# Performance work log

Measured on AMD Instinct MI355X. Metric: run time of the kernel, lower is better.

The kernel has to match this reference:

```python
import jax, jax.numpy as jnp
import numpy as np

EMBED = 1024
HEADS = 16
HEAD_DIM = EMBED // HEADS
WIN = 256  # attention_window w; band width = 2w+1


def setup_inputs() -> dict:
    key = jax.random.key(0)
    ks = jax.random.split(key, 10)
    b, s, e = 2, 4096, EMBED
    scale = 1.0 / np.sqrt(e)
    inp = {"x": jax.random.normal(ks[0], (b, s, e), jnp.float32)}
    for i, (wn, bn) in enumerate([("Wq", "bq"), ("Wk", "bk"), ("Wv", "bv"), ("Wo", "bo")]):
        inp[wn] = jax.random.normal(ks[1 + i], (e, e), jnp.float32) * scale
        inp[bn] = jax.random.normal(ks[5 + i], (e,), jnp.float32) * 0.01
    return inp


def _rope_headaxis(x):
    # Replicates RotaryEmbedding applied to [b, s, h, d]: the original indexes
    # x.shape[2] (== num_heads here), so phase varies over the HEAD axis.
    h, d = x.shape[2], x.shape[3]
    inv = 1.0 / (10000.0 ** (jnp.arange(0, d, 2, dtype=jnp.float32) / d))
    freqs = jnp.arange(h, dtype=jnp.float32)[:, None] * inv[None, :]
    emb = jnp.concatenate([freqs, freqs], axis=-1)  # [h, d]
    cos = jnp.cos(emb)[None, None]  # [1,1,h,d]
    sin = jnp.sin(emb)[None, None]
    x2 = jnp.stack([-x[..., 1::2], x[..., 0::2]], axis=-1).reshape(x.shape)
    return x * cos + x2 * sin


def reference(x, Wq, bq, Wk, bk, Wv, bv, Wo, bo):
    b, s, e = x.shape
    h, d, w = HEADS, HEAD_DIM, WIN
    q = (x @ Wq.T + bq).reshape(b, s, h, d)
    k = (x @ Wk.T + bk).reshape(b, s, h, d)
    v = (x @ Wv.T + bv).reshape(b, s, h, d)
    q = _rope_headaxis(q) / jnp.sqrt(jnp.float32(d))
    k = _rope_headaxis(k)

    # Band (sliding-window) attention: query chunk c of size w attends to key
    # chunks c-1, c, c+1 (3w keys); relative-position + boundary masking makes
    # this identical to the original sliding_chunks band of width 2w+1.
    nc = s // w
    qc = q.reshape(b, nc, w, h, d)
    pad = [(0, 0), (w, w), (0, 0), (0, 0)]
    kp = jnp.pad(k, pad)
    vp = jnp.pad(v, pad)
    idx = jnp.arange(nc)[:, None] * w + jnp.arange(3 * w)[None, :]  # [nc, 3w]
    k3 = kp[:, idx]  # [b, nc, 3w, h, d]
    v3 = vp[:, idx]
    scores = jnp.einsum('bcxhd,bcyhd->bhcxy', qc, k3)  # [b,h,nc,w,3w]

    c = jnp.arange(nc)[:, None, None]
    xq = jnp.arange(w)[None, :, None]
    y = jnp.arange(3 * w)[None, None, :]
    kpos = c * w + y - w  # absolute key position
    valid = (y >= xq) & (y <= xq + 2 * w) & (kpos >= 0) & (kpos < s)
    scores = jnp.where(valid[None, None], scores, -jnp.inf)

    probs = jax.nn.softmax(scores, axis=-1)  # fp32 softmax, as in original
    ctx = jnp.einsum('bhcxy,bcyhd->bcxhd', probs, v3).reshape(b, s, e)
    return ctx @ Wo.T + bo
```

## Files before the change

kernel.cpp:

```cpp
#include <hip/hip_runtime.h>


typedef _Float16 half8 __attribute__((ext_vector_type(8)));
typedef _Float16 half4v __attribute__((ext_vector_type(4)));
typedef float floatx4 __attribute__((ext_vector_type(4)));

typedef __attribute__((address_space(3))) unsigned int lds_u32;
typedef const __attribute__((address_space(1))) unsigned int glb_u32;

__device__ __forceinline__ void async_copy16(const void* g, void* l) {
  __builtin_amdgcn_global_load_lds((glb_u32*)g, (lds_u32*)l, 16, 0, 0);
}

__global__ __launch_bounds__(256) void convert_kernel(
    const float* __restrict__ x, const float* __restrict__ wq,
    const float* __restrict__ wk, const float* __restrict__ wv,
    const float* __restrict__ wo, _Float16* __restrict__ dst) {
  const int e0 = (blockIdx.x * 256 + threadIdx.x) * 4;
  const float* src; int off;
  if      (e0 <  8388608) { src = x;  off = e0; }
  else if (e0 <  9437184) { src = wq; off = e0 -  8388608; }
  else if (e0 < 10485760) { src = wk; off = e0 -  9437184; }
  else if (e0 < 11534336) { src = wv; off = e0 - 10485760; }
  else                    { src = wo; off = e0 - 11534336; }
  const float4 f = *(const float4*)(src + off);
  half4v h;
  h[0] = (_Float16)f.x; h[1] = (_Float16)f.y;
  h[2] = (_Float16)f.z; h[3] = (_Float16)f.w;
  *(half4v*)(dst + e0) = h;
}

__global__ __launch_bounds__(256, 2) void gemm_qkv_kernel(
    const _Float16* __restrict__ A, const _Float16* __restrict__ w0,
    const _Float16* __restrict__ w1, const _Float16* __restrict__ w2,
    const float* __restrict__ b0, const float* __restrict__ b1,
    const float* __restrict__ b2, _Float16* __restrict__ o0,
    _Float16* __restrict__ o1, _Float16* __restrict__ o2) {
  __shared__ _Float16 As[128 * 32];
  __shared__ _Float16 Bs[128 * 32];
  const int tid = threadIdx.x;
  const int w = tid >> 6, lane = tid & 63;
  const int l4 = lane & 15, quad = lane >> 4;
  const int wm = w & 1, wn = w >> 1;
  const int m0 = blockIdx.x * 128, n0 = blockIdx.y * 128;

  const _Float16* B; const float* bias; _Float16* out;
  if (blockIdx.z == 0)      { B = w0; bias = b0; out = o0; }
  else if (blockIdx.z == 1) { B = w1; bias = b1; out = o1; }
  else                      { B = w2; bias = b2; out = o2; }
  const bool dorope = blockIdx.z < 2;
  const float scl = (blockIdx.z == 0) ? 0.18033688f : 1.0f;

  const floatx4 zero = {0.f, 0.f, 0.f, 0.f};
  floatx4 acc[4][4];
#pragma unroll
  for (int i = 0; i < 4; ++i)
#pragma unroll
    for (int j = 0; j < 4; ++j) acc[i][j] = zero;

  const int fcb = (quad ^ ((l4 >> 2) & 3)) * 8;

  for (int kt = 0; kt < 32; ++kt) {
    const int k0 = kt * 32;
#pragma unroll
    for (int i = 0; i < 2; ++i) {
      const int p = i * 256 + tid;
      const int r = p >> 2;
      const int cb = (p & 3) ^ ((r >> 2) & 3);
      async_copy16(A + (m0 + r) * 1024 + k0 + cb * 8, As + (i * 256 + w * 64) * 8);
      async_copy16(B + (n0 + r) * 1024 + k0 + cb * 8, Bs + (i * 256 + w * 64) * 8);
    }
    __syncthreads();
    half8 af[4], bf[4];
#pragma unroll
    for (int mt = 0; mt < 4; ++mt)
      af[mt] = *(const half8*)(As + (wm * 64 + mt * 16 + l4) * 32 + fcb);
#pragma unroll
    for (int nt = 0; nt < 4; ++nt)
      bf[nt] = *(const half8*)(Bs + (wn * 64 + nt * 16 + l4) * 32 + fcb);
#pragma unroll
    for (int mt = 0; mt < 4; ++mt)
#pragma unroll
      for (int nt = 0; nt < 4; ++nt)
        acc[mt][nt] = __builtin_amdgcn_mfma_f32_16x16x32_f16(af[mt], bf[nt], acc[mt][nt], 0, 0, 0);
    __syncthreads();
  }

#pragma unroll
  for (int nt = 0; nt < 4; ++nt) {
    const int n = n0 + wn * 64 + nt * 16 + l4;
    const float bval = bias[n];
    const int hh = n >> 6, dd = n & 63;
    float c_ = 1.f, ss = 0.f;
    if (dorope) {
      const float freq = __expf((float)(n & 31) * -0.28782314f);
      float s_;
      __sincosf((float)hh * freq, &s_, &c_);
      ss = (n & 1) ? s_ : -s_;
    }
#pragma unroll
    for (int mt = 0; mt < 4; ++mt)
#pragma unroll
      for (int r = 0; r < 4; ++r) {
        const int m = m0 + wm * 64 + mt * 16 + quad * 4 + r;
        const int bb = m >> 12, s = m & 4095;
        float val = acc[mt][nt][r] + bval;
        const float prt = __shfl_xor(val, 1);
        if (dorope) val = (val * c_ + prt * ss) * scl;
        out[((bb * 16 + hh) * 4096 + s) * 64 + dd] = (_Float16)val;
      }
  }
}

__global__ __launch_bounds__(256, 2) void gemm_out_kernel(
    const _Float16* __restrict__ A, const _Float16* __restrict__ B,
    const float* __restrict__ bias, float* __restrict__ out) {
  __shared__ _Float16 As[128 * 32];
  __shared__ _Float16 Bs[128 * 32];
  const int tid = threadIdx.x;
  const int w = tid >> 6, lane = tid & 63;
  const int l4 = lane & 15, quad = lane >> 4;
  const int wm = w & 1, wn = w >> 1;
  const int m0 = blockIdx.x * 128, n0 = blockIdx.y * 128;

  const floatx4 zero = {0.f, 0.f, 0.f, 0.f};
  floatx4 acc[4][4];
#pragma unroll
  for (int i = 0; i < 4; ++i)
#pragma unroll
    for (int j = 0; j < 4; ++j) acc[i][j] = zero;

  const int fcb = (quad ^ ((l4 >> 2) & 3)) * 8;

  for (int kt = 0; kt < 32; ++kt) {
    const int k0 = kt * 32;
#pragma unroll
    for (int i = 0; i < 2; ++i) {
      const int p = i * 256 + tid;
      const int r = p >> 2;
      const int cb = (p & 3) ^ ((r >> 2) & 3);
      async_copy16(A + (m0 + r) * 1024 + k0 + cb * 8, As + (i * 256 + w * 64) * 8);
      async_copy16(B + (n0 + r) * 1024 + k0 + cb * 8, Bs + (i * 256 + w * 64) * 8);
    }
    __syncthreads();
    half8 af[4], bf[4];
#pragma unroll
    for (int mt = 0; mt < 4; ++mt)
      af[mt] = *(const half8*)(As + (wm * 64 + mt * 16 + l4) * 32 + fcb);
#pragma unroll
    for (int nt = 0; nt < 4; ++nt)
      bf[nt] = *(const half8*)(Bs + (wn * 64 + nt * 16 + l4) * 32 + fcb);
#pragma unroll
    for (int mt = 0; mt < 4; ++mt)
#pragma unroll
      for (int nt = 0; nt < 4; ++nt)
        acc[mt][nt] = __builtin_amdgcn_mfma_f32_16x16x32_f16(af[mt], bf[nt], acc[mt][nt], 0, 0, 0);
    __syncthreads();
  }

#pragma unroll
  for (int nt = 0; nt < 4; ++nt) {
    const int n = n0 + wn * 64 + nt * 16 + l4;
    const float bval = bias[n];
#pragma unroll
    for (int mt = 0; mt < 4; ++mt)
#pragma unroll
      for (int r = 0; r < 4; ++r) {
        const int m = m0 + wm * 64 + mt * 16 + quad * 4 + r;
        out[m * 1024 + n] = acc[mt][nt][r] + bval;
      }
  }
}

__global__ __launch_bounds__(256) void transpose_v(const _Float16* __restrict__ v,
                                                   _Float16* __restrict__ vt) {
  __shared__ _Float16 tile[64 * 70];
  const int t = threadIdx.x;
  const int bh = blockIdx.y, s0 = blockIdx.x * 64;
  const _Float16* src = v + (bh * 4096 + s0) * 64;
#pragma unroll
  for (int i = 0; i < 2; ++i) {
    const int c = i * 256 + t;
    const int row = c >> 3, cb = c & 7;
    const half8 d = *(const half8*)(src + row * 64 + cb * 8);
#pragma unroll
    for (int u = 0; u < 8; ++u) tile[(cb * 8 + u) * 70 + row] = d[u];
  }
  __syncthreads();
  _Float16* dst = vt + bh * 262144 + s0;
#pragma unroll
  for (int i = 0; i < 2; ++i) {
    const int c = i * 256 + t;
    const int dd = c >> 3, scb = c & 7;
    half8 d;
#pragma unroll
    for (int u = 0; u < 8; ++u) d[u] = tile[dd * 70 + scb * 8 + u];
    *(half8*)(dst + dd * 4096 + scb * 8) = d;
  }
}

__global__ __launch_bounds__(256, 2) void attn_kernel(
    const _Float16* __restrict__ qg, const _Float16* __restrict__ kg,
    const _Float16* __restrict__ vtg, _Float16* __restrict__ ctx) {
  __shared__ _Float16 Ks[128 * 64];
  __shared__ _Float16 Vs[64 * 128];

  const int tid = threadIdx.x;
  const int w = tid >> 6, lane = tid & 63;
  const int l4 = lane & 15, quad = lane >> 4;
  const int q0 = blockIdx.x * 128;
  const int bh = blockIdx.y;
  const _Float16* qbh = qg + bh * 262144;
  const _Float16* kbh = kg + bh * 262144;
  const _Float16* vbh = vtg + bh * 262144;

  half8 qf[2][2];
#pragma unroll
  for (int nt = 0; nt < 2; ++nt)
#pragma unroll
    for (int ks = 0; ks < 2; ++ks)
      qf[nt][ks] = *(const half8*)(qbh + (q0 + w * 32 + nt * 16 + l4) * 64 + ks * 32 + quad * 8);

  const floatx4 zero = {0.f, 0.f, 0.f, 0.f};
  floatx4 OT[4][2];
  float m_st[2], l_st[2];
#pragma unroll
  for (int md = 0; md < 4; ++md)
#pragma unroll
    for (int nt = 0; nt < 2; ++nt) OT[md][nt] = zero;
#pragma unroll
  for (int nt = 0; nt < 2; ++nt) { m_st[nt] = -1e30f; l_st[nt] = 0.f; }

  for (int t = 0; t < 5; ++t) {
    const int kv0 = q0 + (t - 2) * 128;
    if (kv0 < 0 || kv0 >= 4096) continue;

#pragma unroll
    for (int i = 0; i < 4; ++i) {
      const int p = i * 256 + tid;
      const int rk = p >> 3, ck = (p & 7) ^ (rk & 7);
      async_copy16(kbh + (kv0 + rk) * 64 + ck * 8, Ks + (i * 256 + w * 64) * 8);
      const int rv = p >> 4, cv = (p & 15) ^ (rv & 7);
      async_copy16(vbh + rv * 4096 + kv0 + cv * 8, Vs + (i * 256 + w * 64) * 8);
    }
    __syncthreads();

    const bool edge = (t == 0 || t == 4);
#pragma unroll
    for (int hf = 0; hf < 2; ++hf) {
      const int kb = hf * 64;

      floatx4 ST[4][2];
#pragma unroll
      for (int m = 0; m < 4; ++m)
#pragma unroll
        for (int nt = 0; nt < 2; ++nt) ST[m][nt] = zero;
#pragma unroll
      for (int ks = 0; ks < 2; ++ks)
#pragma unroll
        for (int m = 0; m < 4; ++m) {
          const half8 kf = *(const half8*)(Ks + (kb + m * 16 + l4) * 64 +
                                           ((ks * 4 + quad) ^ (l4 & 7)) * 8);
#pragma unroll
          for (int nt = 0; nt < 2; ++nt)
            ST[m][nt] = __builtin_amdgcn_mfma_f32_16x16x32_f16(kf, qf[nt][ks], ST[m][nt], 0, 0, 0);
        }

      if (edge) {
#pragma unroll
        for (int m = 0; m < 4; ++m)
#pragma unroll
          for (int r = 0; r < 4; ++r) {
            const int key = kv0 + kb + m * 16 + quad * 4 + r;
#pragma unroll
            for (int nt = 0; nt < 2; ++nt) {
              const int d = key - (q0 + w * 32 + nt * 16 + l4);
              if (d < -256 || d > 256) ST[m][nt][r] = -1e30f;
            }
          }
      }

#pragma unroll
      for (int nt = 0; nt < 2; ++nt) {
        float mx = -1e30f;
#pragma unroll
        for (int m = 0; m < 4; ++m)
#pragma unroll
          for (int r = 0; r < 4; ++r) mx = fmaxf(mx, ST[m][nt][r]);
        mx = fmaxf(mx, __shfl_xor(mx, 16));
        mx = fmaxf(mx, __shfl_xor(mx, 32));
        const float mnew = fmaxf(m_st[nt], mx);
        const float alpha = exp2f(m_st[nt] - mnew);
        m_st[nt] = mnew;
        float rs = 0.f;
#pragma unroll
        for (int m = 0; m < 4; ++m)
#pragma unroll
          for (int r = 0; r < 4; ++r) {
            const float pv = exp2f(ST[m][nt][r] - mnew);
            ST[m][nt][r] = pv;
            rs += pv;
          }
        rs += __shfl_xor(rs, 16);
        rs += __shfl_xor(rs, 32);
        l_st[nt] = l_st[nt] * alpha + rs;
#pragma unroll
        for (int md = 0; md < 4; ++md)
#pragma unroll
          for (int r = 0; r < 4; ++r) OT[md][nt][r] *= alpha;
      }

#pragma unroll
      for (int m = 0; m < 4; ++m) {
        half4v pb[2];
#pragma unroll
        for (int nt = 0; nt < 2; ++nt) {
          const auto lo = __builtin_amdgcn_cvt_pkrtz(ST[m][nt][0], ST[m][nt][1]);
          const auto hi = __builtin_amdgcn_cvt_pkrtz(ST[m][nt][2], ST[m][nt][3]);
          pb[nt][0] = (_Float16)lo[0]; pb[nt][1] = (_Float16)lo[1];
          pb[nt][2] = (_Float16)hi[0]; pb[nt][3] = (_Float16)hi[1];
        }
#pragma unroll
        for (int md = 0; md < 4; ++md) {
          const half4v vf = *(const half4v*)(Vs + (md * 16 + l4) * 128 +
                                             (((hf * 8 + m * 2 + (quad >> 1)) ^ (l4 & 7)) * 8 +
                                              (quad & 1) * 4));
#pragma unroll
          for (int nt = 0; nt < 2; ++nt)
            OT[md][nt] = __builtin_amdgcn_mfma_f32_16x16x16f16(vf, pb[nt], OT[md][nt], 0, 0, 0);
        }
      }
    }
    __syncthreads();
  }

  const int b = bh >> 4, hh = bh & 15;
#pragma unroll
  for (int nt = 0; nt < 2; ++nt) {
    const float inv_l = 1.f / l_st[nt];
    const int s = q0 + w * 32 + nt * 16 + l4;
#pragma unroll
    for (int md = 0; md < 4; ++md) {
      half4v o;
#pragma unroll
      for (int r = 0; r < 4; ++r) o[r] = (_Float16)(OT[md][nt][r] * inv_l);
      *(half4v*)(ctx + (b * 4096 + s) * 1024 + hh * 64 + md * 16 + quad * 4) = o;
    }
  }
}

extern "C" void kernel_launch(void* const* d_in, const int* in_sizes, int n_in,
                              void* d_out, int out_size, void* d_ws, size_t ws_size,
                              hipStream_t stream) {
  const float* x  = (const float*)d_in[0];
  const float* Wq = (const float*)d_in[1];
  const float* bq = (const float*)d_in[2];
  const float* Wk = (const float*)d_in[3];
  const float* bk = (const float*)d_in[4];
  const float* Wv = (const float*)d_in[5];
  const float* bv = (const float*)d_in[6];
  const float* Wo = (const float*)d_in[7];
  const float* bo = (const float*)d_in[8];

  _Float16* ws   = (_Float16*)d_ws;
  _Float16* xh   = ws;
  _Float16* wqh  = ws + 8388608;
  _Float16* wkh  = ws + 9437184;
  _Float16* wvh  = ws + 10485760;
  _Float16* woh  = ws + 11534336;
  _Float16* qh   = ws + 12582912;
  _Float16* kh   = ws + 20971520;
  _Float16* vh   = ws + 29360128;
  _Float16* vth  = ws + 37748736;
  _Float16* ctxh = xh;

  convert_kernel<<<12288, 256, 0, stream>>>(x, Wq, Wk, Wv, Wo, ws);
  gemm_qkv_kernel<<<dim3(64, 8, 3), 256, 0, stream>>>(xh, wqh, wkh, wvh,
                                                      bq, bk, bv, qh, kh, vh);
  transpose_v<<<dim3(64, 32), 256, 0, stream>>>(vh, vth);
  attn_kernel<<<dim3(32, 32), 256, 0, stream>>>(qh, kh, vth, ctxh);
  gemm_out_kernel<<<dim3(64, 8), 256, 0, stream>>>(ctxh, woh, bo, (float*)d_out);
}
```

Baseline: 258.4 us.

## Deepen GEMM K-tile, remap blocks per XCD, stage QKV epilogue through LDS

Both GEMMs now load 64-wide K slices (16 iterations instead of 32), which halves the barrier count, and use an XOR swizzle sized for 8 chunks. Blocks are linearized and remapped so that each XCD handles a contiguous group of M tiles, to improve L2 reuse of A and B. The QKV epilogue writes its results into padded LDS and then issues coalesced 16-byte stores into the head-major layout, replacing scattered 2-byte stores. LDS use per block grows to about 34 KB, which may limit occupancy.

```diff
diff --git a/kernel.cpp b/kernel.cpp
--- a/kernel.cpp
+++ b/kernel.cpp
@@ -36,20 +36,28 @@
     const float* __restrict__ b0, const float* __restrict__ b1,
     const float* __restrict__ b2, _Float16* __restrict__ o0,
     _Float16* __restrict__ o1, _Float16* __restrict__ o2) {
-  __shared__ _Float16 As[128 * 32];
-  __shared__ _Float16 Bs[128 * 32];
+  __shared__ _Float16 smem[17408];
+  _Float16* As = smem;
+  _Float16* Bs = smem + 8192;
+
   const int tid = threadIdx.x;
   const int w = tid >> 6, lane = tid & 63;
   const int l4 = lane & 15, quad = lane >> 4;
   const int wm = w & 1, wn = w >> 1;
-  const int m0 = blockIdx.x * 128, n0 = blockIdx.y * 128;
+
+  const int bid = blockIdx.x;
+  const int xcd = bid & 7, li = bid >> 3;
+  const int z = li >> 6, r_ = li & 63;
+  const int n_l = r_ >> 3, m_l = r_ & 7;
+  const int m0 = (xcd * 8 + m_l) * 128;
+  const int n0 = n_l * 128;
 
   const _Float16* B; const float* bias; _Float16* out;
-  if (blockIdx.z == 0)      { B = w0; bias = b0; out = o0; }
-  else if (blockIdx.z == 1) { B = w1; bias = b1; out = o1; }
-  else                      { B = w2; bias = b2; out = o2; }
-  const bool dorope = blockIdx.z < 2;
-  const float scl = (blockIdx.z == 0) ? 0.18033688f : 1.0f;
+  if (z == 0)      { B = w0; bias = b0; out = o0; }
+  else if (z == 1) { B = w1; bias = b1; out = o1; }
+  else             { B = w2; bias = b2; out = o2; }
+  const bool dorope = z < 2;
+  const float scl = (z == 0) ? 0.18033688f : 1.0f;
 
   const floatx4 zero = {0.f, 0.f, 0.f, 0.f};
   floatx4 acc[4][4];
@@ -58,39 +66,43 @@
 #pragma unroll
     for (int j = 0; j < 4; ++j) acc[i][j] = zero;
 
-  const int fcb = (quad ^ ((l4 >> 2) & 3)) * 8;
-
-  for (int kt = 0; kt < 32; ++kt) {
-    const int k0 = kt * 32;
-#pragma unroll
-    for (int i = 0; i < 2; ++i) {
+  for (int kt = 0; kt < 16; ++kt) {
+    const int k0 = kt * 64;
+#pragma unroll
+    for (int i = 0; i < 4; ++i) {
       const int p = i * 256 + tid;
-      const int r = p >> 2;
-      const int cb = (p & 3) ^ ((r >> 2) & 3);
-      async_copy16(A + (m0 + r) * 1024 + k0 + cb * 8, As + (i * 256 + w * 64) * 8);
-      async_copy16(B + (n0 + r) * 1024 + k0 + cb * 8, Bs + (i * 256 + w * 64) * 8);
-    }
-    __syncthreads();
-    half8 af[4], bf[4];
-#pragma unroll
-    for (int mt = 0; mt < 4; ++mt)
-      af[mt] = *(const half8*)(As + (wm * 64 + mt * 16 + l4) * 32 + fcb);
-#pragma unroll
-    for (int nt = 0; nt < 4; ++nt)
-      bf[nt] = *(const half8*)(Bs + (wn * 64 + nt * 16 + l4) * 32 + fcb);
-#pragma unroll
-    for (int mt = 0; mt < 4; ++mt)
+      const int r = p >> 3;
+      const int c = (p & 7) ^ (r & 7);
+      async_copy16(A + (m0 + r) * 1024 + k0 + c * 8, As + (i * 256 + w * 64) * 8);
+      async_copy16(B + (n0 + r) * 1024 + k0 + c * 8, Bs + (i * 256 + w * 64) * 8);
+    }
+    __syncthreads();
+#pragma unroll
+    for (int ks = 0; ks < 2; ++ks) {
+      half8 af[4], bf[4];
+#pragma unroll
+      for (int mt = 0; mt < 4; ++mt)
+        af[mt] = *(const half8*)(As + (wm * 64 + mt * 16 + l4) * 64 +
+                                 (((ks * 4 + quad) ^ (l4 & 7)) * 8));
 #pragma unroll
       for (int nt = 0; nt < 4; ++nt)
-        acc[mt][nt] = __builtin_amdgcn_mfma_f32_16x16x32_f16(af[mt], bf[nt], acc[mt][nt], 0, 0, 0);
-    __syncthreads();
-  }
-
+        bf[nt] = *(const half8*)(Bs + (wn * 64 + nt * 16 + l4) * 64 +
+                                 (((ks * 4 + quad) ^ (l4 & 7)) * 8));
+#pragma unroll
+      for (int mt = 0; mt < 4; ++mt)
+#pragma unroll
+        for (int nt = 0; nt < 4; ++nt)
+          acc[mt][nt] = __builtin_amdgcn_mfma_f32_16x16x32_f16(af[mt], bf[nt], acc[mt][nt], 0, 0, 0);
+    }
+    __syncthreads();
+  }
+
+  _Float16* tile = smem;
 #pragma unroll
   for (int nt = 0; nt < 4; ++nt) {
     const int n = n0 + wn * 64 + nt * 16 + l4;
     const float bval = bias[n];
-    const int hh = n >> 6, dd = n & 63;
+    const int hh = n >> 6;
     float c_ = 1.f, ss = 0.f;
     if (dorope) {
       const float freq = __expf((float)(n & 31) * -0.28782314f);
@@ -102,26 +114,42 @@
     for (int mt = 0; mt < 4; ++mt)
 #pragma unroll
       for (int r = 0; r < 4; ++r) {
-        const int m = m0 + wm * 64 + mt * 16 + quad * 4 + r;
-        const int bb = m >> 12, s = m & 4095;
         float val = acc[mt][nt][r] + bval;
         const float prt = __shfl_xor(val, 1);
         if (dorope) val = (val * c_ + prt * ss) * scl;
-        out[((bb * 16 + hh) * 4096 + s) * 64 + dd] = (_Float16)val;
+        tile[(wm * 64 + mt * 16 + quad * 4 + r) * 132 + wn * 64 + nt * 16 + l4] = (_Float16)val;
       }
+  }
+  __syncthreads();
+#pragma unroll
+  for (int j = 0; j < 8; ++j) {
+    const int idx = j * 256 + tid;
+    const int row = idx >> 4, cb = idx & 15;
+    const int n = n0 + cb * 8;
+    const int hh = n >> 6, dd = n & 63;
+    const int m = m0 + row, bb = m >> 12, s = m & 4095;
+    const half8 vals = *(const half8*)(tile + row * 132 + cb * 8);
+    *(half8*)(out + ((bb * 16 + hh) * 4096 + s) * 64 + dd) = vals;
   }
 }
 
 __global__ __launch_bounds__(256, 2) void gemm_out_kernel(
     const _Float16* __restrict__ A, const _Float16* __restrict__ B,
     const float* __restrict__ bias, float* __restrict__ out) {
-  __shared__ _Float16 As[128 * 32];
-  __shared__ _Float16 Bs[128 * 32];
+  __shared__ _Float16 smem[16384];
+  _Float16* As = smem;
+  _Float16* Bs = smem + 8192;
+
   const int tid = threadIdx.x;
   const int w = tid >> 6, lane = tid & 63;
   const int l4 = lane & 15, quad = lane >> 4;
   const int wm = w & 1, wn = w >> 1;
-  const int m0 = blockIdx.x * 128, n0 = blockIdx.y * 128;
+
+  const int bid = blockIdx.x;
+  const int xcd = bid & 7, li = bid >> 3;
+  const int n_l = li >> 3, m_l = li & 7;
+  const int m0 = (xcd * 8 + m_l) * 128;
+  const int n0 = n_l * 128;
 
   const floatx4 zero = {0.f, 0.f, 0.f, 0.f};
   floatx4 acc[4][4];
@@ -130,31 +158,34 @@
 #pragma unroll
     for (int j = 0; j < 4; ++j) acc[i][j] = zero;
 
-  const int fcb = (quad ^ ((l4 >> 2) & 3)) * 8;
-
-  for (int kt = 0; kt < 32; ++kt) {
-    const int k0 = kt * 32;
-#pragma unroll
-    for (int i = 0; i < 2; ++i) {
+  for (int kt = 0; kt < 16; ++kt) {
+    const int k0 = kt * 64;
+#pragma unroll
+    for (int i = 0; i < 4; ++i) {
       const int p = i * 256 + tid;
-      const int r = p >> 2;
-      const int cb = (p & 3) ^ ((r >> 2) & 3);
-      async_copy16(A + (m0 + r) * 1024 + k0 + cb * 8, As + (i * 256 + w * 64) * 8);
-      async_copy16(B + (n0 + r) * 1024 + k0 + cb * 8, Bs + (i * 256 + w * 64) * 8);
-    }
-    __syncthreads();
-    half8 af[4], bf[4];
-#pragma unroll
-    for (int mt = 0; mt < 4; ++mt)
-      af[mt] = *(const half8*)(As + (wm * 64 + mt * 16 + l4) * 32 + fcb);
-#pragma unroll
-    for (int nt = 0; nt < 4; ++nt)
-      bf[nt] = *(const half8*)(Bs + (wn * 64 + nt * 16 + l4) * 32 + fcb);
-#pragma unroll
-    for (int mt = 0; mt < 4; ++mt)
+      const int r = p >> 3;
+      const int c = (p & 7) ^ (r & 7);
+      async_copy16(A + (m0 + r) * 1024 + k0 + c * 8, As + (i * 256 + w * 64) * 8);
+      async_copy16(B + (n0 + r) * 1024 + k0 + c * 8, Bs + (i * 256 + w * 64) * 8);
+    }
+    __syncthreads();
+#pragma unroll
+    for (int ks = 0; ks < 2; ++ks) {
+      half8 af[4], bf[4];
+#pragma unroll
+      for (int mt = 0; mt < 4; ++mt)
+        af[mt] = *(const half8*)(As + (wm * 64 + mt * 16 + l4) * 64 +
+                                 (((ks * 4 + quad) ^ (l4 & 7)) * 8));
 #pragma unroll
       for (int nt = 0; nt < 4; ++nt)
-        acc[mt][nt] = __builtin_amdgcn_mfma_f32_16x16x32_f16(af[mt], bf[nt], acc[mt][nt], 0, 0, 0);
+        bf[nt] = *(const half8*)(Bs + (wn * 64 + nt * 16 + l4) * 64 +
+                                 (((ks * 4 + quad) ^ (l4 & 7)) * 8));
+#pragma unroll
+      for (int mt = 0; mt < 4; ++mt)
+#pragma unroll
+        for (int nt = 0; nt < 4; ++nt)
+          acc[mt][nt] = __builtin_amdgcn_mfma_f32_16x16x32_f16(af[mt], bf[nt], acc[mt][nt], 0, 0, 0);
+    }
     __syncthreads();
   }
 
@@ -375,9 +406,9 @@
   _Float16* ctxh = xh;
 
   convert_kernel<<<12288, 256, 0, stream>>>(x, Wq, Wk, Wv, Wo, ws);
-  gemm_qkv_kernel<<<dim3(64, 8, 3), 256, 0, stream>>>(xh, wqh, wkh, wvh,
-                                                      bq, bk, bv, qh, kh, vh);
+  gemm_qkv_kernel<<<1536, 256, 0, stream>>>(xh, wqh, wkh, wvh,
+                                            bq, bk, bv, qh, kh, vh);
   transpose_v<<<dim3(64, 32), 256, 0, stream>>>(vh, vth);
   attn_kernel<<<dim3(32, 32), 256, 0, stream>>>(qh, kh, vth, ctxh);
-  gemm_out_kernel<<<dim3(64, 8), 256, 0, stream>>>(ctxh, woh, bo, (float*)d_out);
-}
+  gemm_out_kernel<<<512, 256, 0, stream>>>(ctxh, woh, bo, (float*)d_out);
+}
```

Measured after the change: 256.6 us. No clear change (-0.7%).
